# Kernel optimization log

Measured on AMD Instinct MI355X. Metric: run time of the kernel, lower is better.

The kernel has to match this reference:

```python
import jax, jax.numpy as jnp
import numpy as np

N = 50000      # num nodes
EG = 1600000   # num edges (avg degree 32)
IN = 64        # in_dim
OUT = 64       # out_dim
H = 4          # num_heads
D = OUT // H   # per-head dim


def setup_inputs() -> dict:
    key = jax.random.key(0)
    ks = jax.random.split(key, 12)
    s = 1.0 / np.sqrt(IN)
    return {
        "x": jax.random.normal(ks[0], (N, IN), jnp.float32),
        "edge_attr": jax.random.normal(ks[1], (EG, IN), jnp.float32),
        "edge_index": jax.random.randint(ks[2], (2, EG), 0, N, jnp.int32),
        "Wq": jax.random.uniform(ks[3], (OUT, IN), jnp.float32, -s, s),
        "bq": jax.random.uniform(ks[4], (OUT,), jnp.float32, -s, s),
        "Wk": jax.random.uniform(ks[5], (OUT, IN), jnp.float32, -s, s),
        "bk": jax.random.uniform(ks[6], (OUT,), jnp.float32, -s, s),
        "We": jax.random.uniform(ks[7], (OUT, IN), jnp.float32, -s, s),
        "be": jax.random.uniform(ks[8], (OUT,), jnp.float32, -s, s),
        "Wv": jax.random.uniform(ks[9], (OUT, IN), jnp.float32, -s, s),
        "bv": jax.random.uniform(ks[10], (OUT,), jnp.float32, -s, s),
    }


def reference(x, edge_attr, edge_index, Wq, bq, Wk, bk, We, be, Wv, bv):
    n = x.shape[0]
    # linear projections, reshaped to [*, H, D]
    Qh = (x @ Wq.T + bq).reshape(n, H, D)
    Kh = (x @ Wk.T + bk).reshape(n, H, D)
    Vh = (x @ Wv.T + bv).reshape(n, H, D)
    Ee = (edge_attr @ We.T + be).reshape(-1, H, D)
    src = edge_index[0]
    dst = edge_index[1]
    # per-edge score: sum_d K[src] * Q[dst] / sqrt(D) * E  -> [E, H]
    score = ((Kh[src] * Qh[dst]) * (1.0 / np.sqrt(D)) * Ee).sum(-1)
    score = jnp.exp(jnp.clip(score, -5.0, 5.0))            # [E, H]
    msg = Vh[src] * score[..., None]                        # [E, H, D]
    wV = jax.ops.segment_sum(msg, dst, num_segments=n)      # [N, H, D]
    # note: original forward returns wV without dividing by Z
    return wV.reshape(n, H * D)
```

## Files before the change

kernel.cpp:

```cpp
#include <hip/hip_runtime.h>


typedef __attribute__((ext_vector_type(8))) short bf16x8;
typedef __attribute__((ext_vector_type(4))) float f32x4;

union frag_u { uint32_t u[4]; bf16x8 v; };

__device__ __forceinline__ uint32_t pack2(float a, float b) {
    return (__float_as_uint(a) >> 16) | (__float_as_uint(b) & 0xffff0000u);
}

__device__ __forceinline__ void cvt4(float4 v, uint32_t& h0, uint32_t& h1,
                                     uint32_t& l0, uint32_t& l1) {
    float hx = __uint_as_float(__float_as_uint(v.x) & 0xffff0000u);
    float hy = __uint_as_float(__float_as_uint(v.y) & 0xffff0000u);
    float hz = __uint_as_float(__float_as_uint(v.z) & 0xffff0000u);
    float hw = __uint_as_float(__float_as_uint(v.w) & 0xffff0000u);
    h0 = pack2(v.x, v.y);
    h1 = pack2(v.z, v.w);
    l0 = pack2(v.x - hx, v.y - hy);
    l1 = pack2(v.z - hz, v.w - hw);
}

__global__ __launch_bounds__(256) void proj_kernel(
    const float* __restrict__ x,
    const float* __restrict__ Wq, const float* __restrict__ bq,
    const float* __restrict__ Wk, const float* __restrict__ bk,
    const float* __restrict__ Wv, const float* __restrict__ bv,
    float* __restrict__ Qb, float* __restrict__ KV,
    int n)
{
    __shared__ float WqT[64 * 65];
    __shared__ float WkT[64 * 65];
    __shared__ float WvT[64 * 65];
    __shared__ float xs[4][4][64];

    const int tid  = threadIdx.x;
    const int wave = tid >> 6;
    const int lane = tid & 63;

    #pragma unroll
    for (int k = 0; k < 16; ++k) {
        int idx = tid + k * 256;
        int j = idx >> 6, i = idx & 63;
        WqT[i * 65 + j] = Wq[idx];
        WkT[i * 65 + j] = Wk[idx];
        WvT[i * 65 + j] = Wv[idx];
    }
    const float bqv = bq[lane];
    const float bkv = bk[lane];
    const float bvv = bv[lane];
    __syncthreads();

    for (int blockbase = blockIdx.x * 16; blockbase < n;
         blockbase += gridDim.x * 16) {
        int base = blockbase + wave * 4;
        #pragma unroll
        for (int j = 0; j < 4; ++j) {
            int node = base + j;
            xs[wave][j][lane] = (node < n) ? x[node * 64 + lane] : 0.f;
        }
        __syncthreads();

        float accq[4], acck[4], accv[4];
        #pragma unroll
        for (int j = 0; j < 4; ++j) { accq[j] = bqv; acck[j] = bkv; accv[j] = bvv; }

        #pragma unroll
        for (int f = 0; f < 16; ++f) {
            float wq[4], wk[4], wv[4];
            #pragma unroll
            for (int u = 0; u < 4; ++u) {
                int i = 4 * f + u;
                wq[u] = WqT[i * 65 + lane];
                wk[u] = WkT[i * 65 + lane];
                wv[u] = WvT[i * 65 + lane];
            }
            #pragma unroll
            for (int j = 0; j < 4; ++j) {
                float4 xv = *reinterpret_cast<const float4*>(&xs[wave][j][4 * f]);
                accq[j] = fmaf(xv.x, wq[0], accq[j]);
                accq[j] = fmaf(xv.y, wq[1], accq[j]);
                accq[j] = fmaf(xv.z, wq[2], accq[j]);
                accq[j] = fmaf(xv.w, wq[3], accq[j]);
                acck[j] = fmaf(xv.x, wk[0], acck[j]);
                acck[j] = fmaf(xv.y, wk[1], acck[j]);
                acck[j] = fmaf(xv.z, wk[2], acck[j]);
                acck[j] = fmaf(xv.w, wk[3], acck[j]);
                accv[j] = fmaf(xv.x, wv[0], accv[j]);
                accv[j] = fmaf(xv.y, wv[1], accv[j]);
                accv[j] = fmaf(xv.z, wv[2], accv[j]);
                accv[j] = fmaf(xv.w, wv[3], accv[j]);
            }
        }

        #pragma unroll
        for (int j = 0; j < 4; ++j) {
            int node = base + j;
            if (node < n) {
                Qb[(size_t)node * 64 + lane]       = accq[j];
                KV[(size_t)node * 128 + lane]      = acck[j];
                KV[(size_t)node * 128 + 64 + lane] = accv[j];
            }
        }
        __syncthreads();
    }
}

__global__ __launch_bounds__(256) void edge_kernel(
    const float* __restrict__ ea, const int* __restrict__ ei,
    const float* __restrict__ Qb, const float* __restrict__ KV,
    const float* __restrict__ We, const float* __restrict__ be,
    float* __restrict__ out, int EG)
{
    const int tid  = threadIdx.x;
    const int lane = tid & 63;
    const int g    = lane >> 4;
    const int q    = lane & 15;

    frag_u Bh[4][2], Bl[4][2];
    #pragma unroll
    for (int nt = 0; nt < 4; ++nt) {
        #pragma unroll
        for (int ks = 0; ks < 2; ++ks) {
            #pragma unroll
            for (int b = 0; b < 2; ++b) {
                float4 w4 = *reinterpret_cast<const float4*>(
                    &We[(size_t)(16 * nt + q) * 64 + 32 * ks + 16 * b + 4 * g]);
                cvt4(w4, Bh[nt][ks].u[2 * b + 0], Bh[nt][ks].u[2 * b + 1],
                         Bl[nt][ks].u[2 * b + 0], Bl[nt][ks].u[2 * b + 1]);
            }
        }
    }
    float bias[4];
    #pragma unroll
    for (int nt = 0; nt < 4; ++nt) bias[nt] = be[16 * nt + q];

    const int nwaves = gridDim.x * 4;
    const int wid    = blockIdx.x * 4 + (tid >> 6);

    for (int eb = wid * 16; eb < EG; eb += nwaves * 16) {
        const int eld = min(eb + q, EG - 1);
        const int se  = ei[eld];
        const int de  = ei[EG + eld];

        frag_u Ah[2], Al[2];
        const float* arow = &ea[(size_t)eld * 64];
        #pragma unroll
        for (int ks = 0; ks < 2; ++ks) {
            #pragma unroll
            for (int b = 0; b < 2; ++b) {
                float4 a4 = *reinterpret_cast<const float4*>(
                    &arow[32 * ks + 16 * b + 4 * g]);
                cvt4(a4, Ah[ks].u[2 * b + 0], Ah[ks].u[2 * b + 1],
                         Al[ks].u[2 * b + 0], Al[ks].u[2 * b + 1]);
            }
        }

        f32x4 acc[4];
        #pragma unroll
        for (int nt = 0; nt < 4; ++nt) {
            acc[nt][0] = bias[nt]; acc[nt][1] = bias[nt];
            acc[nt][2] = bias[nt]; acc[nt][3] = bias[nt];
            #pragma unroll
            for (int ks = 0; ks < 2; ++ks) {
                acc[nt] = __builtin_amdgcn_mfma_f32_16x16x32_bf16(
                              Al[ks].v, Bh[nt][ks].v, acc[nt], 0, 0, 0);
                acc[nt] = __builtin_amdgcn_mfma_f32_16x16x32_bf16(
                              Ah[ks].v, Bl[nt][ks].v, acc[nt], 0, 0, 0);
                acc[nt] = __builtin_amdgcn_mfma_f32_16x16x32_bf16(
                              Ah[ks].v, Bh[nt][ks].v, acc[nt], 0, 0, 0);
            }
        }

        #pragma unroll
        for (int r = 0; r < 4; ++r) {
            const int srcr = __shfl(se, 4 * g + r);
            const int dstr = __shfl(de, 4 * g + r);
            const bool act = (eb + 4 * g + r) < EG;
            const float* kb = KV + (size_t)srcr * 128 + q;
            const float* qp = Qb + (size_t)dstr * 64 + q;

            float s_[4];
            #pragma unroll
            for (int nt = 0; nt < 4; ++nt) {
                float kv = kb[16 * nt];
                float qv = qp[16 * nt];
                float t  = kv * qv * (0.25f * acc[nt][r]);
                t += __shfl_xor(t, 1);
                t += __shfl_xor(t, 2);
                t += __shfl_xor(t, 4);
                t += __shfl_xor(t, 8);
                t = fminf(fmaxf(t, -5.f), 5.f);
                s_[nt] = __expf(t);
            }
            if (act) {
                float* ob = out + (size_t)dstr * 64 + q;
                #pragma unroll
                for (int nt = 0; nt < 4; ++nt) {
                    float vv = kb[64 + 16 * nt];
                    atomicAdd(&ob[16 * nt], vv * s_[nt]);
                }
            }
        }
    }
}

extern "C" void kernel_launch(void* const* d_in, const int* in_sizes, int n_in,
                              void* d_out, int out_size, void* d_ws, size_t ws_size,
                              hipStream_t stream) {
    const float* x   = (const float*)d_in[0];
    const float* ea  = (const float*)d_in[1];
    const int*   ei  = (const int*)d_in[2];
    const float* Wq  = (const float*)d_in[3];
    const float* bq  = (const float*)d_in[4];
    const float* Wk  = (const float*)d_in[5];
    const float* bk  = (const float*)d_in[6];
    const float* We  = (const float*)d_in[7];
    const float* be  = (const float*)d_in[8];
    const float* Wv  = (const float*)d_in[9];
    const float* bv  = (const float*)d_in[10];
    float* out = (float*)d_out;

    const int n  = in_sizes[0] / 64;
    const int EG = in_sizes[1] / 64;

    float* Qb = (float*)d_ws;
    float* KV = Qb + (size_t)n * 64;

    hipMemsetAsync(d_out, 0, (size_t)out_size * sizeof(float), stream);

    const int projGrid = (n + 15) / 16;
    proj_kernel<<<projGrid, 256, 0, stream>>>(x, Wq, bq, Wk, bk, Wv, bv,
                                              Qb, KV, n);

    const int edgeGrid = 4096;
    edge_kernel<<<edgeGrid, 256, 0, stream>>>(ea, ei, Qb, KV, We, be,
                                              out, EG);
}
```

Measured before the change: 562.6 us.

## Stage We fragments and edge projections in LDS, process one edge per wave-row

The split bf16 We fragments move from per-lane registers into shared memory, with each wave building one slice. The MFMA edge projection results are transposed through LDS so that all 64 lanes work on a single edge at a time. This gives contiguous 64-float gathers of K, V and Q and coalesced atomics per edge, instead of 16-lane strided access. It also loads 16 edge indices per lane, drops the tail clamping (this assumes EG is a multiple of 16), and sets the grid to 2500 blocks so each wave handles exactly 10 tiles.

```diff
diff --git a/kernel.cpp b/kernel.cpp
--- a/kernel.cpp
+++ b/kernel.cpp
@@ -4,7 +4,7 @@
 typedef __attribute__((ext_vector_type(8))) short bf16x8;
 typedef __attribute__((ext_vector_type(4))) float f32x4;
 
-union frag_u { uint32_t u[4]; bf16x8 v; };
+union frag_u { uint32_t u[4]; uint4 u4; bf16x8 v; };
 
 __device__ __forceinline__ uint32_t pack2(float a, float b) {
     return (__float_as_uint(a) >> 16) | (__float_as_uint(b) & 0xffff0000u);
@@ -113,39 +113,49 @@
     const float* __restrict__ We, const float* __restrict__ be,
     float* __restrict__ out, int EG)
 {
+    __shared__ uint4 bfragLDS[16][64];
+    __shared__ float els[4][16][66];
+
     const int tid  = threadIdx.x;
+    const int wave = __builtin_amdgcn_readfirstlane(tid >> 6);
     const int lane = tid & 63;
     const int g    = lane >> 4;
     const int q    = lane & 15;
 
-    frag_u Bh[4][2], Bl[4][2];
-    #pragma unroll
-    for (int nt = 0; nt < 4; ++nt) {
+    {
+        const int nt = wave;
         #pragma unroll
         for (int ks = 0; ks < 2; ++ks) {
+            frag_u fh, fl;
             #pragma unroll
             for (int b = 0; b < 2; ++b) {
                 float4 w4 = *reinterpret_cast<const float4*>(
                     &We[(size_t)(16 * nt + q) * 64 + 32 * ks + 16 * b + 4 * g]);
-                cvt4(w4, Bh[nt][ks].u[2 * b + 0], Bh[nt][ks].u[2 * b + 1],
-                         Bl[nt][ks].u[2 * b + 0], Bl[nt][ks].u[2 * b + 1]);
-            }
-        }
-    }
-    float bias[4];
+                cvt4(w4, fh.u[2 * b + 0], fh.u[2 * b + 1],
+                         fl.u[2 * b + 0], fl.u[2 * b + 1]);
+            }
+            bfragLDS[nt * 4 + ks * 2 + 0][lane] = fh.u4;
+            bfragLDS[nt * 4 + ks * 2 + 1][lane] = fl.u4;
+        }
+    }
+    float bias4[4];
     #pragma unroll
-    for (int nt = 0; nt < 4; ++nt) bias[nt] = be[16 * nt + q];
-
-    const int nwaves = gridDim.x * 4;
-    const int wid    = blockIdx.x * 4 + (tid >> 6);
-
-    for (int eb = wid * 16; eb < EG; eb += nwaves * 16) {
-        const int eld = min(eb + q, EG - 1);
-        const int se  = ei[eld];
-        const int de  = ei[EG + eld];
+    for (int nt = 0; nt < 4; ++nt) bias4[nt] = be[16 * nt + q];
+    __syncthreads();
+
+    const int nw  = gridDim.x * 4;
+    const int wid = blockIdx.x * 4 + wave;
+
+    for (int eb = wid * 16; eb < EG; eb += nw * 16) {
+        int srcs[16], dsts[16];
+        #pragma unroll
+        for (int r = 0; r < 16; ++r) {
+            srcs[r] = ei[eb + r];
+            dsts[r] = ei[EG + eb + r];
+        }
 
         frag_u Ah[2], Al[2];
-        const float* arow = &ea[(size_t)eld * 64];
+        const float* arow = &ea[(size_t)(eb + q) * 64];
         #pragma unroll
         for (int ks = 0; ks < 2; ++ks) {
             #pragma unroll
@@ -160,49 +170,47 @@
         f32x4 acc[4];
         #pragma unroll
         for (int nt = 0; nt < 4; ++nt) {
-            acc[nt][0] = bias[nt]; acc[nt][1] = bias[nt];
-            acc[nt][2] = bias[nt]; acc[nt][3] = bias[nt];
+            acc[nt][0] = bias4[nt]; acc[nt][1] = bias4[nt];
+            acc[nt][2] = bias4[nt]; acc[nt][3] = bias4[nt];
             #pragma unroll
             for (int ks = 0; ks < 2; ++ks) {
+                frag_u bh, bl;
+                bh.u4 = bfragLDS[nt * 4 + ks * 2 + 0][lane];
+                bl.u4 = bfragLDS[nt * 4 + ks * 2 + 1][lane];
                 acc[nt] = __builtin_amdgcn_mfma_f32_16x16x32_bf16(
-                              Al[ks].v, Bh[nt][ks].v, acc[nt], 0, 0, 0);
+                              Al[ks].v, bh.v, acc[nt], 0, 0, 0);
                 acc[nt] = __builtin_amdgcn_mfma_f32_16x16x32_bf16(
-                              Ah[ks].v, Bl[nt][ks].v, acc[nt], 0, 0, 0);
+                              Ah[ks].v, bl.v, acc[nt], 0, 0, 0);
                 acc[nt] = __builtin_amdgcn_mfma_f32_16x16x32_bf16(
-                              Ah[ks].v, Bh[nt][ks].v, acc[nt], 0, 0, 0);
-            }
-        }
-
-        #pragma unroll
-        for (int r = 0; r < 4; ++r) {
-            const int srcr = __shfl(se, 4 * g + r);
-            const int dstr = __shfl(de, 4 * g + r);
-            const bool act = (eb + 4 * g + r) < EG;
-            const float* kb = KV + (size_t)srcr * 128 + q;
-            const float* qp = Qb + (size_t)dstr * 64 + q;
-
-            float s_[4];
-            #pragma unroll
-            for (int nt = 0; nt < 4; ++nt) {
-                float kv = kb[16 * nt];
-                float qv = qp[16 * nt];
-                float t  = kv * qv * (0.25f * acc[nt][r]);
-                t += __shfl_xor(t, 1);
-                t += __shfl_xor(t, 2);
-                t += __shfl_xor(t, 4);
-                t += __shfl_xor(t, 8);
-                t = fminf(fmaxf(t, -5.f), 5.f);
-                s_[nt] = __expf(t);
-            }
-            if (act) {
-                float* ob = out + (size_t)dstr * 64 + q;
-                #pragma unroll
-                for (int nt = 0; nt < 4; ++nt) {
-                    float vv = kb[64 + 16 * nt];
-                    atomicAdd(&ob[16 * nt], vv * s_[nt]);
-                }
-            }
-        }
+                              Ah[ks].v, bh.v, acc[nt], 0, 0, 0);
+            }
+        }
+
+        #pragma unroll
+        for (int nt = 0; nt < 4; ++nt) {
+            #pragma unroll
+            for (int r = 0; r < 4; ++r)
+                els[wave][4 * g + r][16 * nt + q] = acc[nt][r];
+        }
+        __builtin_amdgcn_wave_barrier();
+
+        #pragma unroll
+        for (int r = 0; r < 16; ++r) {
+            const float Ee = els[wave][r][lane];
+            const float* kb = KV + (size_t)srcs[r] * 128;
+            const float kv = kb[lane];
+            const float vv = kb[64 + lane];
+            const float qv = Qb[(size_t)dsts[r] * 64 + lane];
+            float t = kv * qv * 0.25f * Ee;
+            t += __shfl_xor(t, 1);
+            t += __shfl_xor(t, 2);
+            t += __shfl_xor(t, 4);
+            t += __shfl_xor(t, 8);
+            t = fminf(fmaxf(t, -5.f), 5.f);
+            float s = __expf(t);
+            atomicAdd(&out[(size_t)dsts[r] * 64 + lane], vv * s);
+        }
+        __builtin_amdgcn_wave_barrier();
     }
 }
 
@@ -234,7 +242,5 @@
     proj_kernel<<<projGrid, 256, 0, stream>>>(x, Wq, bq, Wk, bk, Wv, bv,
                                               Qb, KV, n);
 
-    const int edgeGrid = 4096;
-    edge_kernel<<<edgeGrid, 256, 0, stream>>>(ea, ei, Qb, KV, We, be,
-                                              out, EG);
-}
+    edge_kernel<<<2500, 256, 0, stream>>>(ea, ei, Qb, KV, We, be, out, EG);
+}
```

New measurement: 503.3 us. 1.12x faster.
